# Kernel optimization log

Measured on AMD Instinct MI355X. Metric: run time of the kernel, lower is better.

## Reference

```python
import jax, jax.numpy as jnp
import numpy as np

N, D = 16384, 512
LOGIT_SCALE = 14.285714  # 1/0.07, standard CLIP temperature


def setup_inputs() -> dict:
    key = jax.random.key(0)
    k1, k2 = jax.random.split(key)
    image_features = jax.random.normal(k1, (N, D), dtype=jnp.float32)
    text_features = jax.random.normal(k2, (N, D), dtype=jnp.float32)
    logit_scale = jnp.asarray(LOGIT_SCALE, dtype=jnp.float32)
    return {
        "image_features": image_features,
        "text_features": text_features,
        "logit_scale": logit_scale,
    }


def reference(image_features, text_features, logit_scale):
    # logits_per_image = scale * img @ txt.T  -> [N, N]
    # logits_per_text is its transpose, so compute the GEMM once.
    logits = logit_scale * jnp.einsum("nd,md->nm", image_features, text_features)
    diag = jnp.diagonal(logits)  # correct-pair logits (labels = arange)
    # cross_entropy with label i on row i: logsumexp(row) - logit[i,i]
    loss_i = jnp.mean(jax.nn.logsumexp(logits, axis=1) - diag)
    # text loss uses transposed logits -> column-wise logsumexp
    loss_t = jnp.mean(jax.nn.logsumexp(logits, axis=0) - diag)
    return (loss_i + loss_t) * 0.5
```

## Files before the change

kernel.cpp:

```cpp
#include <hip/hip_runtime.h>
#include <hip/hip_bf16.h>

#define N_ 16384
#define D_ 512
#define BM 128
#define BN 128
#define BK 64
#define NBLK (N_ / BM)

typedef __attribute__((ext_vector_type(8))) __bf16 bf16x8;
typedef __attribute__((ext_vector_type(4))) float f32x4;

#define GLDS(gptr, lptr)                                                              \
  __builtin_amdgcn_global_load_lds((const __attribute__((address_space(1))) void*)(gptr), \
                                   (__attribute__((address_space(3))) void*)(lptr), 16, 0, 0)

__device__ inline unsigned short f2bf(float f) {
  __hip_bfloat16 h = __float2bfloat16(f);
  return *reinterpret_cast<unsigned short*>(&h);
}

__global__ void cvt_bf16_kernel(const float* __restrict__ src,
                                unsigned short* __restrict__ dst, long n,
                                const float* __restrict__ scale_p) {
  const float s = scale_p ? scale_p[0] : 1.0f;
  long i = ((long)blockIdx.x * blockDim.x + threadIdx.x) * 8;
  const long stride = (long)gridDim.x * blockDim.x * 8;
  typedef __attribute__((ext_vector_type(8))) unsigned short us8;
  for (; i < n; i += stride) {
    const float4* sp = (const float4*)(src + i);
    float4 f0 = sp[0], f1 = sp[1];
    us8 v;
    v[0] = f2bf(f0.x * s); v[1] = f2bf(f0.y * s); v[2] = f2bf(f0.z * s); v[3] = f2bf(f0.w * s);
    v[4] = f2bf(f1.x * s); v[5] = f2bf(f1.y * s); v[6] = f2bf(f1.z * s); v[7] = f2bf(f1.w * s);
    *(us8*)(dst + i) = v;
  }
}

__global__ __launch_bounds__(256, 4)
void gemm_lse_kernel(const unsigned short* __restrict__ A,
                     const unsigned short* __restrict__ B,
                     float2* __restrict__ rowMS,
                     float2* __restrict__ colMS,
                     float* __restrict__ diag) {
  __shared__ unsigned short As[BM][BK];
  __shared__ unsigned short Bs[BN][BK];
  __shared__ float rowbuf[2][BM][2];
  __shared__ float colbuf[2][BN][2];

  const int t = threadIdx.x;
  const int l = t & 63;
  const int wid = t >> 6;
  const int wr = wid >> 1;
  const int wc = wid & 1;

  int id = blockIdx.x;
  id = (id & 7) * (NBLK * NBLK / 8) + (id >> 3);
  const int br = id / NBLK;
  const int bc = id % NBLK;

  const int srow = t >> 3;
  const int scol = (((t & 7) ^ (srow & 7)) << 3);

  f32x4 acc[4][4];
#pragma unroll
  for (int m = 0; m < 4; ++m)
#pragma unroll
    for (int n = 0; n < 4; ++n) acc[m][n] = (f32x4)0.0f;

  const unsigned short* aBase = A + (size_t)(br * BM + srow) * D_ + scol;
  const unsigned short* bBase = B + (size_t)(bc * BN + srow) * D_ + scol;
  char* asBase = (char*)&As[0][0] + t * 16;
  char* bsBase = (char*)&Bs[0][0] + t * 16;

  const int swz = (l & 7) << 4;

  for (int kt = 0; kt < D_ / BK; ++kt) {
    const int k0 = kt * BK;
#pragma unroll
    for (int c = 0; c < 4; ++c) GLDS(aBase + k0 + c * 32 * D_, asBase + c * 4096);
#pragma unroll
    for (int c = 0; c < 4; ++c) GLDS(bBase + k0 + c * 32 * D_, bsBase + c * 4096);
    __syncthreads();
#pragma unroll
    for (int kk = 0; kk < 2; ++kk) {
      const int cb = (kk * 64 + (l >> 4) * 16);
      bf16x8 af[4], bfv[4];
#pragma unroll
      for (int m = 0; m < 4; ++m)
        af[m] = *(const bf16x8*)((const char*)&As[0][0] +
                                 (wr * 64 + m * 16 + (l & 15)) * 128 + (cb ^ swz));
#pragma unroll
      for (int n = 0; n < 4; ++n)
        bfv[n] = *(const bf16x8*)((const char*)&Bs[0][0] +
                                  (wc * 64 + n * 16 + (l & 15)) * 128 + (cb ^ swz));
#pragma unroll
      for (int m = 0; m < 4; ++m)
#pragma unroll
        for (int n = 0; n < 4; ++n)
          acc[m][n] = __builtin_amdgcn_mfma_f32_16x16x32_bf16(af[m], bfv[n], acc[m][n], 0, 0, 0);
    }
    __syncthreads();
  }

  if (br == bc && wr == wc) {
#pragma unroll
    for (int m = 0; m < 4; ++m)
#pragma unroll
      for (int r = 0; r < 4; ++r)
        if ((l & 15) == ((l >> 4) * 4 + r))
          diag[br * BM + wr * 64 + m * 16 + (l & 15)] = acc[m][m][r];
  }

#pragma unroll
  for (int m = 0; m < 4; ++m) {
#pragma unroll
    for (int r = 0; r < 4; ++r) {
      float mx = fmaxf(fmaxf(acc[m][0][r], acc[m][1][r]), fmaxf(acc[m][2][r], acc[m][3][r]));
#pragma unroll
      for (int off = 1; off < 16; off <<= 1) mx = fmaxf(mx, __shfl_xor(mx, off, 64));
      float s = 0.f;
#pragma unroll
      for (int n = 0; n < 4; ++n) s += __expf(acc[m][n][r] - mx);
#pragma unroll
      for (int off = 1; off < 16; off <<= 1) s += __shfl_xor(s, off, 64);
      if ((l & 15) == 0) {
        int row = wr * 64 + m * 16 + (l >> 4) * 4 + r;
        rowbuf[wc][row][0] = mx;
        rowbuf[wc][row][1] = s;
      }
    }
  }

#pragma unroll
  for (int n = 0; n < 4; ++n) {
    float mx = -1e30f;
#pragma unroll
    for (int m = 0; m < 4; ++m)
#pragma unroll
      for (int r = 0; r < 4; ++r) mx = fmaxf(mx, acc[m][n][r]);
    mx = fmaxf(mx, __shfl_xor(mx, 16, 64));
    mx = fmaxf(mx, __shfl_xor(mx, 32, 64));
    float s = 0.f;
#pragma unroll
    for (int m = 0; m < 4; ++m)
#pragma unroll
      for (int r = 0; r < 4; ++r) s += __expf(acc[m][n][r] - mx);
    s += __shfl_xor(s, 16, 64);
    s += __shfl_xor(s, 32, 64);
    if ((l >> 4) == 0) {
      int col = wc * 64 + n * 16 + l;
      colbuf[wr][col][0] = mx;
      colbuf[wr][col][1] = s;
    }
  }
  __syncthreads();

  if (t < BM) {
    float m0 = rowbuf[0][t][0], s0 = rowbuf[0][t][1];
    float m1 = rowbuf[1][t][0], s1 = rowbuf[1][t][1];
    float mm = fmaxf(m0, m1);
    float ss = s0 * __expf(m0 - mm) + s1 * __expf(m1 - mm);
    rowMS[(size_t)bc * N_ + br * BM + t] = make_float2(mm, ss);
  } else {
    int c = t - BM;
    float m0 = colbuf[0][c][0], s0 = colbuf[0][c][1];
    float m1 = colbuf[1][c][0], s1 = colbuf[1][c][1];
    float mm = fmaxf(m0, m1);
    float ss = s0 * __expf(m0 - mm) + s1 * __expf(m1 - mm);
    colMS[(size_t)br * N_ + bc * BN + c] = make_float2(mm, ss);
  }
}

__global__ void reduce1_kernel(const float2* __restrict__ rowMS,
                               const float2* __restrict__ colMS,
                               const float* __restrict__ diag,
                               float* __restrict__ partials) {
  const int tid = blockIdx.x * blockDim.x + threadIdx.x;
  float m = -1e30f, s = 0.f;
  if (tid < N_) {
    const int r = tid;
    for (int cb = 0; cb < NBLK; ++cb) {
      float2 p = rowMS[(size_t)cb * N_ + r];
      float nm = fmaxf(m, p.x);
      s = s * __expf(m - nm) + p.y * __expf(p.x - nm);
      m = nm;
    }
    m = m + logf(s) - diag[r];
  } else {
    const int c = tid - N_;
    for (int rb = 0; rb < NBLK; ++rb) {
      float2 p = colMS[(size_t)rb * N_ + c];
      float nm = fmaxf(m, p.x);
      s = s * __expf(m - nm) + p.y * __expf(p.x - nm);
      m = nm;
    }
    m = m + logf(s) - diag[c];
  }
  float val = m;
#pragma unroll
  for (int off = 1; off < 64; off <<= 1) val += __shfl_xor(val, off, 64);
  __shared__ float red[4];
  if ((threadIdx.x & 63) == 0) red[threadIdx.x >> 6] = val;
  __syncthreads();
  if (threadIdx.x == 0) partials[blockIdx.x] = red[0] + red[1] + red[2] + red[3];
}

__global__ void reduce2_kernel(const float* __restrict__ partials, float* __restrict__ out) {
  const int t = threadIdx.x;
  float v = partials[t] + partials[t + 64];
#pragma unroll
  for (int off = 1; off < 64; off <<= 1) v += __shfl_xor(v, off, 64);
  if (t == 0) out[0] = v * (1.0f / (2.0f * (float)N_));
}

extern "C" void kernel_launch(void* const* d_in, const int* in_sizes, int n_in,
                              void* d_out, int out_size, void* d_ws, size_t ws_size,
                              hipStream_t stream) {
  const float* img = (const float*)d_in[0];
  const float* txt = (const float*)d_in[1];
  const float* scale = (const float*)d_in[2];
  float* out = (float*)d_out;

  char* ws = (char*)d_ws;
  size_t off = 0;
  unsigned short* imgB = (unsigned short*)(ws + off); off += (size_t)N_ * D_ * 2;
  unsigned short* txtB = (unsigned short*)(ws + off); off += (size_t)N_ * D_ * 2;
  float2* rowMS = (float2*)(ws + off); off += (size_t)NBLK * N_ * sizeof(float2);
  float2* colMS = (float2*)(ws + off); off += (size_t)NBLK * N_ * sizeof(float2);
  float* diag = (float*)(ws + off); off += (size_t)N_ * sizeof(float);
  float* partials = (float*)(ws + off); off += 128 * sizeof(float);
  (void)ws_size; (void)in_sizes; (void)n_in; (void)out_size;

  cvt_bf16_kernel<<<1024, 256, 0, stream>>>(img, imgB, (long)N_ * D_, scale);
  cvt_bf16_kernel<<<1024, 256, 0, stream>>>(txt, txtB, (long)N_ * D_, nullptr);
  gemm_lse_kernel<<<NBLK * NBLK, 256, 0, stream>>>(imgB, txtB, rowMS, colMS, diag);
  reduce1_kernel<<<(2 * N_) / 256, 256, 0, stream>>>(rowMS, colMS, diag, partials);
  reduce2_kernel<<<1, 64, 0, stream>>>(partials, out);
}
```

Baseline: 408.7 us.

## Use base-2 exponent domain, alias LSE buffers onto tile LDS, raise occupancy

Folds log2(e) into the image-feature bf16 conversion so every exp becomes a native exp2 and the final loss is rescaled by ln2. The row/column max-sum scratch buffers are now aliased onto the As tile in shared memory, cutting LDS per block so launch_bounds can go from 4 to 5 blocks per CU. The block-to-tile mapping is also changed so that groups of blocks share a row tile and sweep a column band. Occupancy gains depend on register pressure fitting the tighter bound, and any register spills would cost speed.

```diff
diff --git a/kernel.cpp b/kernel.cpp
--- a/kernel.cpp
+++ b/kernel.cpp
@@ -6,6 +6,7 @@
 #define BM 128
 #define BN 128
 #define BK 64
+#define NT (D_ / BK)
 #define NBLK (N_ / BM)
 
 typedef __attribute__((ext_vector_type(8))) __bf16 bf16x8;
@@ -15,6 +16,8 @@
   __builtin_amdgcn_global_load_lds((const __attribute__((address_space(1))) void*)(gptr), \
                                    (__attribute__((address_space(3))) void*)(lptr), 16, 0, 0)
 
+#define MFMA16(a, b, c) __builtin_amdgcn_mfma_f32_16x16x32_bf16((a), (b), (c), 0, 0, 0)
+
 __device__ inline unsigned short f2bf(float f) {
   __hip_bfloat16 h = __float2bfloat16(f);
   return *reinterpret_cast<unsigned short*>(&h);
@@ -23,7 +26,7 @@
 __global__ void cvt_bf16_kernel(const float* __restrict__ src,
                                 unsigned short* __restrict__ dst, long n,
                                 const float* __restrict__ scale_p) {
-  const float s = scale_p ? scale_p[0] : 1.0f;
+  const float s = scale_p ? scale_p[0] * 1.4426950408889634f : 1.0f;
   long i = ((long)blockIdx.x * blockDim.x + threadIdx.x) * 8;
   const long stride = (long)gridDim.x * blockDim.x * 8;
   typedef __attribute__((ext_vector_type(8))) unsigned short us8;
@@ -37,16 +40,14 @@
   }
 }
 
-__global__ __launch_bounds__(256, 4)
+__global__ __launch_bounds__(256, 5)
 void gemm_lse_kernel(const unsigned short* __restrict__ A,
                      const unsigned short* __restrict__ B,
                      float2* __restrict__ rowMS,
                      float2* __restrict__ colMS,
                      float* __restrict__ diag) {
-  __shared__ unsigned short As[BM][BK];
-  __shared__ unsigned short Bs[BN][BK];
-  __shared__ float rowbuf[2][BM][2];
-  __shared__ float colbuf[2][BN][2];
+  __shared__ __align__(16) unsigned short As[BM][BK];
+  __shared__ __align__(16) unsigned short Bs[BN][BK];
 
   const int t = threadIdx.x;
   const int l = t & 63;
@@ -54,28 +55,28 @@
   const int wr = wid >> 1;
   const int wc = wid & 1;
 
-  int id = blockIdx.x;
-  id = (id & 7) * (NBLK * NBLK / 8) + (id >> 3);
-  const int br = id / NBLK;
-  const int bc = id % NBLK;
+  const int id = blockIdx.x;
+  const int w = id >> 3;
+  const int bc = (id & 7) * 16 + (w & 15);
+  const int br = w >> 4;
 
   const int srow = t >> 3;
   const int scol = (((t & 7) ^ (srow & 7)) << 3);
-
-  f32x4 acc[4][4];
-#pragma unroll
-  for (int m = 0; m < 4; ++m)
-#pragma unroll
-    for (int n = 0; n < 4; ++n) acc[m][n] = (f32x4)0.0f;
 
   const unsigned short* aBase = A + (size_t)(br * BM + srow) * D_ + scol;
   const unsigned short* bBase = B + (size_t)(bc * BN + srow) * D_ + scol;
   char* asBase = (char*)&As[0][0] + t * 16;
   char* bsBase = (char*)&Bs[0][0] + t * 16;
 
+  f32x4 acc[4][4];
+#pragma unroll
+  for (int m = 0; m < 4; ++m)
+#pragma unroll
+    for (int n = 0; n < 4; ++n) acc[m][n] = (f32x4)0.0f;
+
   const int swz = (l & 7) << 4;
 
-  for (int kt = 0; kt < D_ / BK; ++kt) {
+  for (int kt = 0; kt < NT; ++kt) {
     const int k0 = kt * BK;
 #pragma unroll
     for (int c = 0; c < 4; ++c) GLDS(aBase + k0 + c * 32 * D_, asBase + c * 4096);
@@ -98,10 +99,13 @@
       for (int m = 0; m < 4; ++m)
 #pragma unroll
         for (int n = 0; n < 4; ++n)
-          acc[m][n] = __builtin_amdgcn_mfma_f32_16x16x32_bf16(af[m], bfv[n], acc[m][n], 0, 0, 0);
+          acc[m][n] = MFMA16(af[m], bfv[n], acc[m][n]);
     }
     __syncthreads();
   }
+
+  float* rowbuf = (float*)&As[0][0];
+  float* colbuf = rowbuf + 2 * 128 * 2;
 
   if (br == bc && wr == wc) {
 #pragma unroll
@@ -121,13 +125,13 @@
       for (int off = 1; off < 16; off <<= 1) mx = fmaxf(mx, __shfl_xor(mx, off, 64));
       float s = 0.f;
 #pragma unroll
-      for (int n = 0; n < 4; ++n) s += __expf(acc[m][n][r] - mx);
+      for (int n = 0; n < 4; ++n) s += exp2f(acc[m][n][r] - mx);
 #pragma unroll
       for (int off = 1; off < 16; off <<= 1) s += __shfl_xor(s, off, 64);
       if ((l & 15) == 0) {
-        int row = wr * 64 + m * 16 + (l >> 4) * 4 + r;
-        rowbuf[wc][row][0] = mx;
-        rowbuf[wc][row][1] = s;
+        const int row = wr * 64 + m * 16 + (l >> 4) * 4 + r;
+        rowbuf[(wc * 128 + row) * 2 + 0] = mx;
+        rowbuf[(wc * 128 + row) * 2 + 1] = s;
       }
     }
   }
@@ -145,29 +149,29 @@
 #pragma unroll
     for (int m = 0; m < 4; ++m)
 #pragma unroll
-      for (int r = 0; r < 4; ++r) s += __expf(acc[m][n][r] - mx);
+      for (int r = 0; r < 4; ++r) s += exp2f(acc[m][n][r] - mx);
     s += __shfl_xor(s, 16, 64);
     s += __shfl_xor(s, 32, 64);
     if ((l >> 4) == 0) {
-      int col = wc * 64 + n * 16 + l;
-      colbuf[wr][col][0] = mx;
-      colbuf[wr][col][1] = s;
+      const int col = wc * 64 + n * 16 + l;
+      colbuf[(wr * 128 + col) * 2 + 0] = mx;
+      colbuf[(wr * 128 + col) * 2 + 1] = s;
     }
   }
   __syncthreads();
 
   if (t < BM) {
-    float m0 = rowbuf[0][t][0], s0 = rowbuf[0][t][1];
-    float m1 = rowbuf[1][t][0], s1 = rowbuf[1][t][1];
+    float m0 = rowbuf[(0 * 128 + t) * 2 + 0], s0 = rowbuf[(0 * 128 + t) * 2 + 1];
+    float m1 = rowbuf[(1 * 128 + t) * 2 + 0], s1 = rowbuf[(1 * 128 + t) * 2 + 1];
     float mm = fmaxf(m0, m1);
-    float ss = s0 * __expf(m0 - mm) + s1 * __expf(m1 - mm);
+    float ss = s0 * exp2f(m0 - mm) + s1 * exp2f(m1 - mm);
     rowMS[(size_t)bc * N_ + br * BM + t] = make_float2(mm, ss);
   } else {
-    int c = t - BM;
-    float m0 = colbuf[0][c][0], s0 = colbuf[0][c][1];
-    float m1 = colbuf[1][c][0], s1 = colbuf[1][c][1];
+    const int c = t - BM;
+    float m0 = colbuf[(0 * 128 + c) * 2 + 0], s0 = colbuf[(0 * 128 + c) * 2 + 1];
+    float m1 = colbuf[(1 * 128 + c) * 2 + 0], s1 = colbuf[(1 * 128 + c) * 2 + 1];
     float mm = fmaxf(m0, m1);
-    float ss = s0 * __expf(m0 - mm) + s1 * __expf(m1 - mm);
+    float ss = s0 * exp2f(m0 - mm) + s1 * exp2f(m1 - mm);
     colMS[(size_t)br * N_ + bc * BN + c] = make_float2(mm, ss);
   }
 }
@@ -183,19 +187,19 @@
     for (int cb = 0; cb < NBLK; ++cb) {
       float2 p = rowMS[(size_t)cb * N_ + r];
       float nm = fmaxf(m, p.x);
-      s = s * __expf(m - nm) + p.y * __expf(p.x - nm);
+      s = s * exp2f(m - nm) + p.y * exp2f(p.x - nm);
       m = nm;
     }
-    m = m + logf(s) - diag[r];
+    m = m + log2f(s) - diag[r];
   } else {
     const int c = tid - N_;
     for (int rb = 0; rb < NBLK; ++rb) {
       float2 p = colMS[(size_t)rb * N_ + c];
       float nm = fmaxf(m, p.x);
-      s = s * __expf(m - nm) + p.y * __expf(p.x - nm);
+      s = s * exp2f(m - nm) + p.y * exp2f(p.x - nm);
       m = nm;
     }
-    m = m + logf(s) - diag[c];
+    m = m + log2f(s) - diag[c];
   }
   float val = m;
 #pragma unroll
@@ -211,7 +215,7 @@
   float v = partials[t] + partials[t + 64];
 #pragma unroll
   for (int off = 1; off < 64; off <<= 1) v += __shfl_xor(v, off, 64);
-  if (t == 0) out[0] = v * (1.0f / (2.0f * (float)N_));
+  if (t == 0) out[0] = v * (0.69314718055994531f / (2.0f * (float)N_));
 }
 
 extern "C" void kernel_launch(void* const* d_in, const int* in_sizes, int n_in,
```

New measurement: 681.8 us. 1.67x slower.
